# Optimization experiments

Hardware: AMD Instinct MI355X
Metric: run time of the kernel (lower is better)

The kernel has to match this reference:

```python
import jax, jax.numpy as jnp
import numpy as np

N, C, H, W = 64, 512, 32, 32
HID, NCLS = 240, 10


def setup_inputs() -> dict:
    key = jax.random.key(0)
    ks = jax.random.split(key, 6)
    d = {
        "x": jax.random.normal(ks[0], (N, C, H, W), jnp.float32),
        "bn1_g": jnp.ones((C,), jnp.float32),
        "bn1_b": jnp.zeros((C,), jnp.float32),
        "bn1_m": jnp.zeros((C,), jnp.float32),
        "bn1_v": jnp.ones((C,), jnp.float32),
        "conv1_w": jax.random.normal(ks[1], (C, C, 3, 3), jnp.float32) * 0.02,
        "bn2_g": jnp.ones((C,), jnp.float32),
        "bn2_b": jnp.zeros((C,), jnp.float32),
        "bn2_m": jnp.zeros((C,), jnp.float32),
        "bn2_v": jnp.ones((C,), jnp.float32),
        "conv2_w": jax.random.normal(ks[2], (C, C, 3, 3), jnp.float32) * 0.02,
        "fc1_w": jax.random.normal(ks[3], (HID, C), jnp.float32) * 0.05,
        "fc1_b": jnp.zeros((HID,), jnp.float32),
        "fc2_w": jax.random.normal(ks[4], (NCLS, HID), jnp.float32) * 0.05,
        "fc2_b": jnp.zeros((NCLS,), jnp.float32),
    }
    return d


def _bn(x, g, b, m, v, eps=1e-5):
    # eval-mode BatchNorm2d, NCHW
    inv = g / jnp.sqrt(v + eps)
    return x * inv[None, :, None, None] + (b - m * inv)[None, :, None, None]


def _conv3(x, w):
    return jax.lax.conv_general_dilated(
        x, w, window_strides=(1, 1), padding="SAME",
        dimension_numbers=("NCHW", "OIHW", "NCHW"))


def _probe(feat, fc1_w, fc1_b, fc2_w, fc2_b):
    # Global_Avg_Flatten -> Linear -> Softplus(beta=5) -> Linear
    g = feat.mean(axis=(2, 3))                       # (N, C)
    h = jax.nn.softplus(5.0 * (g @ fc1_w.T + fc1_b)) / 5.0  # (N, HID)
    return h @ fc2_w.T + fc2_b                       # (N, NCLS)


def _get_mask(feat, fc1_w, fc1_b, fc2_w, fc2_b):
    # eval branch: sum of top-1 + top-2 logits, grad wrt (detached) feat
    feat_sg = jax.lax.stop_gradient(feat)

    def logit_sum(f_):
        logits = _probe(f_, fc1_w, fc1_b, fc2_w, fc2_b)
        idx = jax.lax.top_k(logits, 2)[1]            # (N, 2) int indices
        return jnp.take_along_axis(logits, idx, axis=1).sum()

    g = jax.grad(logit_sum)(feat_sg)                 # (N, C, H, W)
    # adaptive_avg_pool2d(.,1)*H*W == spatial sum
    s = g.sum(axis=(2, 3))                           # (N, C)
    m = jax.nn.softmax(s, axis=1) * 2.0
    return m[:, :, None, None]


def reference(x, bn1_g, bn1_b, bn1_m, bn1_v, conv1_w,
              bn2_g, bn2_b, bn2_m, bn2_v, conv2_w,
              fc1_w, fc1_b, fc2_w, fc2_b):
    out1 = jax.nn.relu(_bn(x, bn1_g, bn1_b, bn1_m, bn1_v))  # equalInOut path
    mask = _get_mask(out1, fc1_w, fc1_b, fc2_w, fc2_b)
    pred_probe = _probe(out1, fc1_w, fc1_b, fc2_w, fc2_b)
    masked = out1 * mask
    h = jax.nn.relu(_bn(_conv3(masked, conv1_w), bn2_g, bn2_b, bn2_m, bn2_v))
    h = _conv3(h, conv2_w)
    out = x + h
    return (out, pred_probe)
```

## Files before the change

kernel.cpp:

```cpp
#include <hip/hip_runtime.h>
#include <stdint.h>

typedef __bf16 bf16x8 __attribute__((ext_vector_type(8)));
typedef float f32x4v __attribute__((ext_vector_type(4)));

typedef __attribute__((address_space(1))) const void gconst_t;
typedef __attribute__((address_space(3))) void lds_t;

#define GLL16(gp, sp) __builtin_amdgcn_global_load_lds((gconst_t*)(uintptr_t)(gp), (lds_t*)(uintptr_t)(sp), 16, 0, 0)

__device__ __forceinline__ unsigned short f2bf(float f) {
  unsigned int u = __float_as_uint(f);
  u = (u + 0x7FFFu + ((u >> 16) & 1u)) >> 16;
  return (unsigned short)u;
}
__device__ __forceinline__ float bf2f(unsigned int b) {
  return __uint_as_float(b << 16);
}

#define SPP 1156

__global__ __launch_bounds__(512) void bnprep(
    const float* __restrict__ g1, const float* __restrict__ b1,
    const float* __restrict__ m1, const float* __restrict__ v1,
    const float* __restrict__ g2, const float* __restrict__ b2,
    const float* __restrict__ m2, const float* __restrict__ v2,
    float* __restrict__ bnp) {
  int t = threadIdx.x;
  float i1 = g1[t] * rsqrtf(v1[t] + 1e-5f);
  bnp[t] = i1;
  bnp[512 + t] = b1[t] - m1[t] * i1;
  float i2 = g2[t] * rsqrtf(v2[t] + 1e-5f);
  bnp[1024 + t] = i2;
  bnp[1536 + t] = b2[t] - m2[t] * i2;
}

__global__ __launch_bounds__(256) void ring_zero(unsigned short* __restrict__ Ap,
                                                 unsigned short* __restrict__ Hp) {
  const int n = blockIdx.y;
  const int p = blockIdx.x * 4 + (threadIdx.x >> 6);
  const int lane = threadIdx.x & 63;
  int y, x;
  if (p < 34) { y = 0; x = p; }
  else if (p < 68) { y = 33; x = p - 34; }
  else if (p < 100) { y = p - 67; x = 0; }
  else { y = p - 99; x = 33; }
  const uint4 z = {0u, 0u, 0u, 0u};
  const size_t off = ((size_t)((n * 34 + y) * 34 + x)) * 512 + lane * 8;
  *(uint4*)(Ap + off) = z;
  *(uint4*)(Hp + off) = z;
}

__global__ __launch_bounds__(256) void wtrans(const float* __restrict__ w1, const float* __restrict__ w2,
                                              unsigned short* __restrict__ w1t, unsigned short* __restrict__ w2t) {
  unsigned e = blockIdx.x * 256u + threadIdx.x;
  if (e >= 4718592u) return;
  const float* w = (e < 2359296u) ? w1 : w2;
  unsigned short* o = (e < 2359296u) ? w1t : w2t;
  unsigned r = (e < 2359296u) ? e : (e - 2359296u);
  unsigned ci = r & 511u, co = (r >> 9) & 511u, tt = r >> 18;
  o[r] = f2bf(w[(co * 512u + ci) * 9u + tt]);
}

__global__ __launch_bounds__(256) void bn1_relu_stage(const float* __restrict__ x, const float* __restrict__ bnp,
                                                      unsigned short* __restrict__ Ap, float* __restrict__ partial) {
  int bid = blockIdx.x;
  int n = bid >> 6, ciblk = (bid >> 3) & 7, yblk = bid & 7;
  int ci0 = ciblk * 64, y0 = yblk * 4;
  int t = threadIdx.x;
  __shared__ __align__(16) float vals[64 * 128];
  __shared__ float ivs[64], bbs[64];
  if (t < 64) { ivs[t] = bnp[ci0 + t]; bbs[t] = bnp[512 + ci0 + t]; }
  __syncthreads();
#pragma unroll
  for (int i = 0; i < 8; ++i) {
    int f4 = i * 256 + t;
    int cil = f4 >> 5, xq = f4 & 31;
    const float* src = x + ((size_t)(n * 512 + ci0 + cil)) * 1024 + y0 * 32 + xq * 4;
    f32x4v v = *(const f32x4v*)src;
    float iv = ivs[cil], bb = bbs[cil];
    f32x4v r;
    r[0] = fmaxf(fmaf(v[0], iv, bb), 0.f);
    r[1] = fmaxf(fmaf(v[1], iv, bb), 0.f);
    r[2] = fmaxf(fmaf(v[2], iv, bb), 0.f);
    r[3] = fmaxf(fmaf(v[3], iv, bb), 0.f);
    *(f32x4v*)&vals[cil * 128 + xq * 4] = r;
  }
  __syncthreads();
  {
    int cil = t >> 2, q = t & 3;
    float s = 0.f;
#pragma unroll
    for (int j = 0; j < 32; ++j) s += vals[cil * 128 + q * 32 + j];
    s += __shfl_xor(s, 1);
    s += __shfl_xor(s, 2);
    if (q == 0) partial[((size_t)n * 512 + ci0 + cil) * 8 + yblk] = s;
  }
  {
    int yx = t >> 1, half = t & 1;
    int y = y0 + (yx >> 5), xx = yx & 31;
    unsigned short* dp = Ap + ((size_t)((n * 34 + y + 1) * 34 + (xx + 1))) * 512 + ci0 + half * 32;
    unsigned wrd[16];
#pragma unroll
    for (int j = 0; j < 16; ++j) {
      unsigned lo = f2bf(vals[(half * 32 + 2 * j) * 128 + yx]);
      unsigned hi = f2bf(vals[(half * 32 + 2 * j + 1) * 128 + yx]);
      wrd[j] = lo | (hi << 16);
    }
#pragma unroll
    for (int k = 0; k < 4; ++k) {
      uint4 u;
      u.x = wrd[k * 4]; u.y = wrd[k * 4 + 1]; u.z = wrd[k * 4 + 2]; u.w = wrd[k * 4 + 3];
      *(uint4*)(dp + k * 8) = u;
    }
  }
}

__global__ __launch_bounds__(256) void probe_mask(const float* __restrict__ partial,
                                                  const float* __restrict__ fc1w, const float* __restrict__ fc1b,
                                                  const float* __restrict__ fc2w, const float* __restrict__ fc2b,
                                                  float* __restrict__ maskp, float* __restrict__ probeout) {
  int n = blockIdx.x, t = threadIdx.x;
  int lane = t & 63, wv = t >> 6;
  __shared__ float gl[512], sl[512], zl[240], hl[240], dzl[240], logl[10], red[4];
  __shared__ int idx2[2];
  for (int c = t; c < 512; c += 256) {
    const float* pp = partial + ((size_t)n * 512 + c) * 8;
    float s = 0.f;
#pragma unroll
    for (int j = 0; j < 8; ++j) s += pp[j];
    gl[c] = s * (1.f / 1024.f);
  }
  __syncthreads();
  if (t < 240) {
    float z = fc1b[t];
    const float* wr = fc1w + t * 512;
    for (int c = 0; c < 512; ++c) z = fmaf(gl[c], wr[c], z);
    zl[t] = z;
    float u = 5.f * z;
    float sp = (u > 20.f) ? u : log1pf(expf(u));
    hl[t] = sp * 0.2f;
  }
  __syncthreads();
  if (t < 10) {
    float L = fc2b[t];
    const float* wr = fc2w + t * 240;
    for (int h = 0; h < 240; ++h) L = fmaf(hl[h], wr[h], L);
    logl[t] = L;
    probeout[n * 10 + t] = L;
  }
  __syncthreads();
  if (t == 0) {
    float b1v = -1e30f, b2v = -1e30f; int i1 = 0, i2 = 0;
    for (int j = 0; j < 10; ++j) {
      float v = logl[j];
      if (v > b1v) { b2v = b1v; i2 = i1; b1v = v; i1 = j; }
      else if (v > b2v) { b2v = v; i2 = j; }
    }
    idx2[0] = i1; idx2[1] = i2;
  }
  __syncthreads();
  if (t < 240) {
    float dh = fc2w[idx2[0] * 240 + t] + fc2w[idx2[1] * 240 + t];
    float u = 5.f * zl[t];
    float sg = 1.f / (1.f + expf(-u));
    dzl[t] = dh * sg;
  }
  __syncthreads();
  for (int c = t; c < 512; c += 256) {
    float s = 0.f;
    for (int h = 0; h < 240; ++h) s = fmaf(dzl[h], fc1w[h * 512 + c], s);
    sl[c] = s;
  }
  __syncthreads();
  float m = fmaxf(sl[t], sl[t + 256]);
#pragma unroll
  for (int o = 32; o > 0; o >>= 1) m = fmaxf(m, __shfl_xor(m, o));
  if (lane == 0) red[wv] = m;
  __syncthreads();
  float mx = fmaxf(fmaxf(red[0], red[1]), fmaxf(red[2], red[3]));
  float e0 = expf(sl[t] - mx), e1 = expf(sl[t + 256] - mx);
  float sum = e0 + e1;
#pragma unroll
  for (int o = 32; o > 0; o >>= 1) sum += __shfl_xor(sum, o);
  __syncthreads();
  if (lane == 0) red[wv] = sum;
  __syncthreads();
  float inv = 2.f / (red[0] + red[1] + red[2] + red[3]);
  maskp[(size_t)n * 512 + t] = e0 * inv;
  maskp[(size_t)n * 512 + t + 256] = e1 * inv;
}

__global__ __launch_bounds__(256) void apply_mask(unsigned short* __restrict__ Ap, const float* __restrict__ maskp) {
  int n = blockIdx.y;
  size_t off = (size_t)n * (SPP * 512) + (size_t)blockIdx.x * 2048 + threadIdx.x * 8;
  int ci0 = (int)(threadIdx.x * 8) & 511;
  uint4 v = *(uint4*)(Ap + off);
  const float* mp = maskp + n * 512 + ci0;
  unsigned r0, r1;
  r0 = f2bf(bf2f(v.x & 0xFFFFu) * mp[0]); r1 = f2bf(bf2f(v.x >> 16) * mp[1]); v.x = r0 | (r1 << 16);
  r0 = f2bf(bf2f(v.y & 0xFFFFu) * mp[2]); r1 = f2bf(bf2f(v.y >> 16) * mp[3]); v.y = r0 | (r1 << 16);
  r0 = f2bf(bf2f(v.z & 0xFFFFu) * mp[4]); r1 = f2bf(bf2f(v.z >> 16) * mp[5]); v.z = r0 | (r1 << 16);
  r0 = f2bf(bf2f(v.w & 0xFFFFu) * mp[6]); r1 = f2bf(bf2f(v.w >> 16) * mp[7]); v.w = r0 | (r1 << 16);
  *(uint4*)(Ap + off) = v;
}

#define LT(M) ((l4 ^ (((M) + l7) & 7)) << 4)

#define RD_A2(QM, H, TAP) do {                                                \
  const int _S0 = ((QM) * 2 + (H) + (TAP) / 3) * 34 + (TAP) % 3;              \
  const int _l = l15x128 + LT(_S0 & 7);                                       \
  const char* _p = ldsAW + _S0 * 128;                                         \
  a2[0][0] = *(const bf16x8*)(_p + _l);                                       \
  a2[0][1] = *(const bf16x8*)(_p + (_l ^ 64));                                \
  a2[1][0] = *(const bf16x8*)(_p + 2048 + _l);                                \
  a2[1][1] = *(const bf16x8*)(_p + 2048 + (_l ^ 64));                         \
} while (0)

#define RD_B(BUF) do {                                                        \
  const char* _pb = ldsb + 49152 + (BUF) * 16384;                             \
  b[0][0] = *(const bf16x8*)(_pb + bRdC);                                     \
  b[0][1] = *(const bf16x8*)(_pb + (bRdC ^ 64));                              \
  b[1][0] = *(const bf16x8*)(_pb + 2048 + bRdC);                              \
  b[1][1] = *(const bf16x8*)(_pb + 2048 + (bRdC ^ 64));                       \
} while (0)

#define ST_B(BUF, BP) do {                                                    \
  GLL16((BP) + bOff0,         ldsb + 49152 + (BUF) * 16384 + tb);             \
  GLL16((BP) + bOff0 + 32768, ldsb + 49152 + (BUF) * 16384 + 8192 + tb);      \
} while (0)

#define ST_A3(AP) do {                                                        \
  GLL16((AP) + aOff0,          ldsb + tb);                                    \
  GLL16((AP) + aOff0 + 32768,  ldsb + 8192 + tb);                             \
  GLL16((AP) + aOff0 + 65536,  ldsb + 16384 + tb);                            \
  GLL16((AP) + aOff0 + 98304,  ldsb + 24576 + tb);                            \
  GLL16((AP) + aOff0 + 131072, ldsb + 32768 + tb);                            \
  GLL16((AP) + aOff0 + 163840, ldsb + 40960 + tb);                            \
} while (0)

#define MFMA8(QM, H) do {                                                     \
  _Pragma("unroll") for (int m = 0; m < 2; ++m)                               \
  _Pragma("unroll") for (int n2 = 0; n2 < 2; ++n2) {                          \
    acc[QM][(H) * 2 + m][n2] = __builtin_amdgcn_mfma_f32_16x16x32_bf16(       \
        a2[m][0], b[n2][0], acc[QM][(H) * 2 + m][n2], 0, 0, 0);               \
    acc[QM][(H) * 2 + m][n2] = __builtin_amdgcn_mfma_f32_16x16x32_bf16(       \
        a2[m][1], b[n2][1], acc[QM][(H) * 2 + m][n2], 0, 0, 0); }             \
} while (0)

#define BARR __builtin_amdgcn_s_barrier()
#define LGKM0 do { asm volatile("s_waitcnt lgkmcnt(0)" ::: "memory");         \
                   __builtin_amdgcn_sched_barrier(0); } while (0)
#define VM0 asm volatile("s_waitcnt vmcnt(0)" ::: "memory")
#define PRIO1 __builtin_amdgcn_s_setprio(1)
#define PRIO0 __builtin_amdgcn_s_setprio(0)

#define TAPSTEP(TAP, PAR) do {                                                \
  const unsigned short* _bpn;                                                 \
  if ((TAP) < 8) _bpn = Wt + (size_t)((TAP) + 1) * 262144 + k8 * 64;          \
  else           _bpn = (k8 < 7) ? Wt + (size_t)(k8 + 1) * 64                 \
                                 : Wt + (size_t)8 * 262144 + 7 * 64;          \
  ST_B((((TAP) + (PAR)) & 1) ^ 1, _bpn);                                      \
  RD_B(((TAP) + (PAR)) & 1);                                                  \
  RD_A2(0, 0, TAP); PRIO1; MFMA8(0, 0); PRIO0;                                \
  RD_A2(0, 1, TAP); PRIO1; MFMA8(0, 1); PRIO0;                                \
  RD_A2(1, 0, TAP); PRIO1; MFMA8(1, 0); PRIO0;                                \
  if ((TAP) < 8) {                                                            \
    RD_A2(1, 1, TAP); PRIO1; MFMA8(1, 1); PRIO0;                              \
    VM0; LGKM0; BARR;                                                         \
  } else {                                                                    \
    RD_A2(1, 1, TAP);                                                         \
    LGKM0; BARR;                                                              \
    if (k8 < 7) { ST_A3(Ag + (size_t)(k8 + 1) * 64); }                        \
    PRIO1; MFMA8(1, 1); PRIO0;                                                \
    VM0; BARR;                                                                \
  }                                                                           \
} while (0)

#define TAP9(PAR)                                                             \
  TAPSTEP(0, PAR); TAPSTEP(1, PAR); TAPSTEP(2, PAR);                          \
  TAPSTEP(3, PAR); TAPSTEP(4, PAR); TAPSTEP(5, PAR);                          \
  TAPSTEP(6, PAR); TAPSTEP(7, PAR); TAPSTEP(8, PAR);

template <int MODE>
__global__ __attribute__((amdgpu_flat_work_group_size(512, 512), amdgpu_waves_per_eu(4, 4)))
void conv256(
    const unsigned short* __restrict__ Ain,
    const unsigned short* __restrict__ Wt,
    const float* __restrict__ bnp,
    unsigned short* __restrict__ Hout,
    const float* __restrict__ xres,
    float* __restrict__ outp) {
  __shared__ __align__(16) char ldsb[81920];

  const int t = threadIdx.x;
  const int lane = t & 63;
  const int wv = t >> 6;
  const int wm = wv >> 2;
  const int wn = wv & 3;

  const int bid = blockIdx.x;
  const int logical = (bid & 7) * 128 + (bid >> 3);
  const int nt = logical & 3, mt = logical >> 2;
  const int n = mt >> 2, yblk = mt & 3;
  const int co0 = nt * 128;

  const unsigned short* Ag = Ain + (size_t)n * (SPP * 512);

  const int kq8 = ((t & 7) ^ ((t >> 3) & 7)) * 8;
  const int aOff0 = (yblk * 272 + (t >> 3)) * 512 + kq8;
  const int bOff0 = (co0 + (t >> 3)) * 512 + kq8;
  const int tb = t * 16;
  const int l4 = lane >> 4, l7 = lane & 7;
  const int l15x128 = (lane & 15) * 128;
  const char* ldsAW = ldsb + wm * 17408;
  const int bRdC = (wn * 32 + (lane & 15)) * 128 + (((lane >> 4) ^ (lane & 7)) << 4);

  bf16x8 a2[2][2];
  bf16x8 b[2][2];
  f32x4v acc[2][4][2];
  const f32x4v zero = {0.f, 0.f, 0.f, 0.f};
#pragma unroll
  for (int qm = 0; qm < 2; ++qm)
#pragma unroll
    for (int mi = 0; mi < 4; ++mi)
#pragma unroll
      for (int ni = 0; ni < 2; ++ni) acc[qm][mi][ni] = zero;

  {
    ST_A3(Ag);
    ST_B(0, Wt);
    VM0; BARR;
  }

  for (int k2 = 0; k2 < 4; ++k2) {
    {
      const int k8 = 2 * k2;
      TAP9(0)
    }
    {
      const int k8 = 2 * k2 + 1;
      TAP9(1)
    }
  }
  VM0;
  __syncthreads();

  if constexpr (MODE == 1) {
#pragma unroll
    for (int ni = 0; ni < 2; ++ni) {
      const int cog = co0 + wn * 32 + ni * 16 + (lane & 15);
      const float iv = bnp[1024 + cog];
      const float bb = bnp[1536 + cog];
#pragma unroll
      for (int qm = 0; qm < 2; ++qm)
#pragma unroll
        for (int mi = 0; mi < 4; ++mi)
#pragma unroll
          for (int r = 0; r < 4; ++r) {
            const int row = wm * 128 + qm * 64 + mi * 16 + (lane >> 4) * 4 + r;
            const int y = yblk * 8 + (row >> 5), xx = row & 31;
            const float v = fmaxf(fmaf(acc[qm][mi][ni][r], iv, bb), 0.f);
            Hout[((size_t)((n * 34 + y + 1) * 34 + (xx + 1))) * 512 + cog] = f2bf(v);
          }
    }
  } else {
    float* sm = (float*)ldsb;
    const int spat0 = yblk * 256;
#pragma unroll 1
    for (int h = 0; h < 4; ++h) {
      if (wn == h) {
#pragma unroll
        for (int ni = 0; ni < 2; ++ni)
#pragma unroll
          for (int qm = 0; qm < 2; ++qm)
#pragma unroll
            for (int mi = 0; mi < 4; ++mi)
#pragma unroll
              for (int r = 0; r < 4; ++r)
                sm[(ni * 16 + (lane & 15)) * 264 +
                   wm * 128 + qm * 64 + mi * 16 + (lane >> 4) * 4 + r] = acc[qm][mi][ni][r];
      }
      __syncthreads();
#pragma unroll
      for (int j = 0; j < 4; ++j) {
        const int c = j * 512 + t;
        const int cc = c >> 6, px = (c & 63) * 4;
        f32x4v v = *(const f32x4v*)&sm[cc * 264 + px];
        const int cog = co0 + h * 32 + cc;
        const size_t o = ((size_t)(n * 512 + cog)) * 1024 + spat0 + px;
        const f32x4v xr = *(const f32x4v*)(xres + o);
        v = v + xr;
        *(f32x4v*)(outp + o) = v;
      }
      __syncthreads();
    }
  }
}

extern "C" void kernel_launch(void* const* d_in, const int* in_sizes, int n_in,
                              void* d_out, int out_size, void* d_ws, size_t ws_size,
                              hipStream_t stream) {
  (void)in_sizes; (void)n_in; (void)out_size; (void)ws_size;
  const float* x    = (const float*)d_in[0];
  const float* bn1g = (const float*)d_in[1];
  const float* bn1b = (const float*)d_in[2];
  const float* bn1m = (const float*)d_in[3];
  const float* bn1v = (const float*)d_in[4];
  const float* w1   = (const float*)d_in[5];
  const float* bn2g = (const float*)d_in[6];
  const float* bn2b = (const float*)d_in[7];
  const float* bn2m = (const float*)d_in[8];
  const float* bn2v = (const float*)d_in[9];
  const float* w2   = (const float*)d_in[10];
  const float* fc1w = (const float*)d_in[11];
  const float* fc1b = (const float*)d_in[12];
  const float* fc2w = (const float*)d_in[13];
  const float* fc2b = (const float*)d_in[14];

  float* out = (float*)d_out;
  float* probeo = out + (size_t)64 * 512 * 32 * 32;

  char* ws = (char*)d_ws;
  unsigned short* Ap  = (unsigned short*)(ws);
  unsigned short* Hp  = (unsigned short*)(ws + 75759616);
  unsigned short* W1t = (unsigned short*)(ws + 151519232);
  unsigned short* W2t = (unsigned short*)(ws + 156237824);
  float* partial      = (float*)(ws + 160956416);
  float* maskp        = (float*)(ws + 162004992);
  float* bnp          = (float*)(ws + 162136064);

  bnprep<<<1, 512, 0, stream>>>(bn1g, bn1b, bn1m, bn1v, bn2g, bn2b, bn2m, bn2v, bnp);
  ring_zero<<<dim3(33, 64), 256, 0, stream>>>(Ap, Hp);
  wtrans<<<18432, 256, 0, stream>>>(w1, w2, W1t, W2t);
  bn1_relu_stage<<<4096, 256, 0, stream>>>(x, bnp, Ap, partial);
  probe_mask<<<64, 256, 0, stream>>>(partial, fc1w, fc1b, fc2w, fc2b, maskp, probeo);
  apply_mask<<<dim3(289, 64), 256, 0, stream>>>(Ap, maskp);
  conv256<1><<<1024, 512, 0, stream>>>(Ap, W1t, bnp, Hp, nullptr, nullptr);
  conv256<2><<<1024, 512, 0, stream>>>(Hp, W2t, bnp, nullptr, x, out);
}
```

Baseline: 578.4 us.

## Switch conv MFMA tiling from 16x16x32 to 32x32x16 bf16 instructions

The implicit-GEMM conv kernel now uses 32x32x16 bf16 MFMAs with four 16-wide accumulators per wave instead of sixteen 16x16 tiles. Each wave covers four image rows of 32 pixels by 32 output channels, and one B fragment is reused across four A fragments per K step. The aim is fewer LDS reads per MFMA and fewer, larger matrix instructions. The LDS swizzle, accumulator layout and both epilogues are rewritten to match. The transpose scratch stride changes to 265 floats, which breaks 16-byte alignment of the vector reads in the residual epilogue.

```diff
diff --git a/kernel.cpp b/kernel.cpp
--- a/kernel.cpp
+++ b/kernel.cpp
@@ -3,6 +3,7 @@
 
 typedef __bf16 bf16x8 __attribute__((ext_vector_type(8)));
 typedef float f32x4v __attribute__((ext_vector_type(4)));
+typedef float f32x16 __attribute__((ext_vector_type(16)));
 
 typedef __attribute__((address_space(1))) const void gconst_t;
 typedef __attribute__((address_space(3))) void lds_t;
@@ -205,25 +206,12 @@
   *(uint4*)(Ap + off) = v;
 }
 
-#define LT(M) ((l4 ^ (((M) + l7) & 7)) << 4)
-
-#define RD_A2(QM, H, TAP) do {                                                \
-  const int _S0 = ((QM) * 2 + (H) + (TAP) / 3) * 34 + (TAP) % 3;              \
-  const int _l = l15x128 + LT(_S0 & 7);                                       \
-  const char* _p = ldsAW + _S0 * 128;                                         \
-  a2[0][0] = *(const bf16x8*)(_p + _l);                                       \
-  a2[0][1] = *(const bf16x8*)(_p + (_l ^ 64));                                \
-  a2[1][0] = *(const bf16x8*)(_p + 2048 + _l);                                \
-  a2[1][1] = *(const bf16x8*)(_p + 2048 + (_l ^ 64));                         \
-} while (0)
-
-#define RD_B(BUF) do {                                                        \
-  const char* _pb = ldsb + 49152 + (BUF) * 16384;                             \
-  b[0][0] = *(const bf16x8*)(_pb + bRdC);                                     \
-  b[0][1] = *(const bf16x8*)(_pb + (bRdC ^ 64));                              \
-  b[1][0] = *(const bf16x8*)(_pb + 2048 + bRdC);                              \
-  b[1][1] = *(const bf16x8*)(_pb + 2048 + (bRdC ^ 64));                       \
-} while (0)
+#define BARR __builtin_amdgcn_s_barrier()
+#define LGKM0 do { asm volatile("s_waitcnt lgkmcnt(0)" ::: "memory");         \
+                   __builtin_amdgcn_sched_barrier(0); } while (0)
+#define VM0 asm volatile("s_waitcnt vmcnt(0)" ::: "memory")
+#define PRIO1 __builtin_amdgcn_s_setprio(1)
+#define PRIO0 __builtin_amdgcn_s_setprio(0)
 
 #define ST_B(BUF, BP) do {                                                    \
   GLL16((BP) + bOff0,         ldsb + 49152 + (BUF) * 16384 + tb);             \
@@ -239,48 +227,69 @@
   GLL16((AP) + aOff0 + 163840, ldsb + 40960 + tb);                            \
 } while (0)
 
-#define MFMA8(QM, H) do {                                                     \
-  _Pragma("unroll") for (int m = 0; m < 2; ++m)                               \
-  _Pragma("unroll") for (int n2 = 0; n2 < 2; ++n2) {                          \
-    acc[QM][(H) * 2 + m][n2] = __builtin_amdgcn_mfma_f32_16x16x32_bf16(       \
-        a2[m][0], b[n2][0], acc[QM][(H) * 2 + m][n2], 0, 0, 0);               \
-    acc[QM][(H) * 2 + m][n2] = __builtin_amdgcn_mfma_f32_16x16x32_bf16(       \
-        a2[m][1], b[n2][1], acc[QM][(H) * 2 + m][n2], 0, 0, 0); }             \
-} while (0)
-
-#define BARR __builtin_amdgcn_s_barrier()
-#define LGKM0 do { asm volatile("s_waitcnt lgkmcnt(0)" ::: "memory");         \
-                   __builtin_amdgcn_sched_barrier(0); } while (0)
-#define VM0 asm volatile("s_waitcnt vmcnt(0)" ::: "memory")
-#define PRIO1 __builtin_amdgcn_s_setprio(1)
-#define PRIO0 __builtin_amdgcn_s_setprio(0)
-
-#define TAPSTEP(TAP, PAR) do {                                                \
-  const unsigned short* _bpn;                                                 \
-  if ((TAP) < 8) _bpn = Wt + (size_t)((TAP) + 1) * 262144 + k8 * 64;          \
-  else           _bpn = (k8 < 7) ? Wt + (size_t)(k8 + 1) * 64                 \
-                                 : Wt + (size_t)8 * 262144 + 7 * 64;          \
+#define MFMA_KK(TAP, BUF, K) do {                                             \
+  const bf16x8 _bf = *(const bf16x8*)(ldsB + (BUF) * 16384 + (bT ^ ((K) << 5))); \
+  const int _Sa = ((TAP) / 3) * 34 + (TAP) % 3;                               \
+  const bf16x8 _a0 = *(const bf16x8*)(ldsAW + (_Sa + 0) * 128 + (aT[(_Sa + 0) & 7] ^ ((K) << 5)));   \
+  const bf16x8 _a1 = *(const bf16x8*)(ldsAW + (_Sa + 34) * 128 + (aT[(_Sa + 34) & 7] ^ ((K) << 5))); \
+  const bf16x8 _a2 = *(const bf16x8*)(ldsAW + (_Sa + 68) * 128 + (aT[(_Sa + 68) & 7] ^ ((K) << 5))); \
+  const bf16x8 _a3 = *(const bf16x8*)(ldsAW + (_Sa + 102) * 128 + (aT[(_Sa + 102) & 7] ^ ((K) << 5))); \
+  acc0 = __builtin_amdgcn_mfma_f32_32x32x16_bf16(_a0, _bf, acc0, 0, 0, 0);    \
+  acc1 = __builtin_amdgcn_mfma_f32_32x32x16_bf16(_a1, _bf, acc1, 0, 0, 0);    \
+  acc2 = __builtin_amdgcn_mfma_f32_32x32x16_bf16(_a2, _bf, acc2, 0, 0, 0);    \
+  acc3 = __builtin_amdgcn_mfma_f32_32x32x16_bf16(_a3, _bf, acc3, 0, 0, 0);    \
+} while (0)
+
+#define TS(TAP, PAR) do {                                                     \
+  const unsigned short* _bpn = Wt + (size_t)((TAP) + 1) * 262144 + k8 * 64;   \
   ST_B((((TAP) + (PAR)) & 1) ^ 1, _bpn);                                      \
-  RD_B(((TAP) + (PAR)) & 1);                                                  \
-  RD_A2(0, 0, TAP); PRIO1; MFMA8(0, 0); PRIO0;                                \
-  RD_A2(0, 1, TAP); PRIO1; MFMA8(0, 1); PRIO0;                                \
-  RD_A2(1, 0, TAP); PRIO1; MFMA8(1, 0); PRIO0;                                \
-  if ((TAP) < 8) {                                                            \
-    RD_A2(1, 1, TAP); PRIO1; MFMA8(1, 1); PRIO0;                              \
-    VM0; LGKM0; BARR;                                                         \
-  } else {                                                                    \
-    RD_A2(1, 1, TAP);                                                         \
+  PRIO1;                                                                      \
+  MFMA_KK(TAP, ((TAP) + (PAR)) & 1, 0);                                       \
+  MFMA_KK(TAP, ((TAP) + (PAR)) & 1, 1);                                       \
+  MFMA_KK(TAP, ((TAP) + (PAR)) & 1, 2);                                       \
+  MFMA_KK(TAP, ((TAP) + (PAR)) & 1, 3);                                       \
+  PRIO0;                                                                      \
+  VM0; LGKM0; BARR;                                                           \
+} while (0)
+
+#define TS_LAST(PAR) do {                                                     \
+  const unsigned short* _bpn = (k8 < 7) ? Wt + (size_t)(k8 + 1) * 64          \
+                                        : Wt + (size_t)8 * 262144 + 7 * 64;   \
+  ST_B(((8 + (PAR)) & 1) ^ 1, _bpn);                                          \
+  PRIO1;                                                                      \
+  MFMA_KK(8, (8 + (PAR)) & 1, 0);                                             \
+  MFMA_KK(8, (8 + (PAR)) & 1, 1);                                             \
+  MFMA_KK(8, (8 + (PAR)) & 1, 2);                                             \
+  PRIO0;                                                                      \
+  {                                                                           \
+    const int _Sa = 2 * 34 + 2;                                               \
+    const bf16x8 _bf = *(const bf16x8*)(ldsB + ((8 + (PAR)) & 1) * 16384 + (bT ^ (3 << 5))); \
+    const bf16x8 _a0 = *(const bf16x8*)(ldsAW + (_Sa + 0) * 128 + (aT[(_Sa + 0) & 7] ^ (3 << 5)));   \
+    const bf16x8 _a1 = *(const bf16x8*)(ldsAW + (_Sa + 34) * 128 + (aT[(_Sa + 34) & 7] ^ (3 << 5))); \
+    const bf16x8 _a2 = *(const bf16x8*)(ldsAW + (_Sa + 68) * 128 + (aT[(_Sa + 68) & 7] ^ (3 << 5))); \
+    const bf16x8 _a3 = *(const bf16x8*)(ldsAW + (_Sa + 102) * 128 + (aT[(_Sa + 102) & 7] ^ (3 << 5))); \
     LGKM0; BARR;                                                              \
     if (k8 < 7) { ST_A3(Ag + (size_t)(k8 + 1) * 64); }                        \
-    PRIO1; MFMA8(1, 1); PRIO0;                                                \
+    PRIO1;                                                                    \
+    acc0 = __builtin_amdgcn_mfma_f32_32x32x16_bf16(_a0, _bf, acc0, 0, 0, 0);  \
+    acc1 = __builtin_amdgcn_mfma_f32_32x32x16_bf16(_a1, _bf, acc1, 0, 0, 0);  \
+    acc2 = __builtin_amdgcn_mfma_f32_32x32x16_bf16(_a2, _bf, acc2, 0, 0, 0);  \
+    acc3 = __builtin_amdgcn_mfma_f32_32x32x16_bf16(_a3, _bf, acc3, 0, 0, 0);  \
+    PRIO0;                                                                    \
     VM0; BARR;                                                                \
   }                                                                           \
 } while (0)
 
 #define TAP9(PAR)                                                             \
-  TAPSTEP(0, PAR); TAPSTEP(1, PAR); TAPSTEP(2, PAR);                          \
-  TAPSTEP(3, PAR); TAPSTEP(4, PAR); TAPSTEP(5, PAR);                          \
-  TAPSTEP(6, PAR); TAPSTEP(7, PAR); TAPSTEP(8, PAR);
+  TS(0, PAR); TS(1, PAR); TS(2, PAR); TS(3, PAR);                             \
+  TS(4, PAR); TS(5, PAR); TS(6, PAR); TS(7, PAR); TS_LAST(PAR);
+
+#define EPI_T(ACC, MF) do {                                                   \
+  _Pragma("unroll") for (int r = 0; r < 16; ++r) {                            \
+    const int xx = (r & 3) + 8 * (r >> 2) + 4 * hi;                           \
+    sm[lx * 265 + ((wm * 4 + (MF)) * 32 + xx)] = ACC[r];                      \
+  }                                                                           \
+} while (0)
 
 template <int MODE>
 __global__ __attribute__((amdgpu_flat_work_group_size(512, 512), amdgpu_waves_per_eu(4, 4)))
@@ -291,13 +300,15 @@
     unsigned short* __restrict__ Hout,
     const float* __restrict__ xres,
     float* __restrict__ outp) {
-  __shared__ __align__(16) char ldsb[81920];
+  __shared__ __align__(128) char ldsb[81920];
 
   const int t = threadIdx.x;
   const int lane = t & 63;
   const int wv = t >> 6;
   const int wm = wv >> 2;
   const int wn = wv & 3;
+  const int lx = lane & 31;
+  const int hi = lane >> 5;
 
   const int bid = blockIdx.x;
   const int logical = (bid & 7) * 128 + (bid >> 3);
@@ -311,21 +322,19 @@
   const int aOff0 = (yblk * 272 + (t >> 3)) * 512 + kq8;
   const int bOff0 = (co0 + (t >> 3)) * 512 + kq8;
   const int tb = t * 16;
-  const int l4 = lane >> 4, l7 = lane & 7;
-  const int l15x128 = (lane & 15) * 128;
+
+  int aT[8];
+#pragma unroll
+  for (int m = 0; m < 8; ++m)
+    aT[m] = lx * 128 + ((hi ^ ((m + lx) & 7)) << 4);
+  const int bT = (wn * 32 + lx) * 128 + ((hi ^ (lx & 7)) << 4);
   const char* ldsAW = ldsb + wm * 17408;
-  const int bRdC = (wn * 32 + (lane & 15)) * 128 + (((lane >> 4) ^ (lane & 7)) << 4);
-
-  bf16x8 a2[2][2];
-  bf16x8 b[2][2];
-  f32x4v acc[2][4][2];
-  const f32x4v zero = {0.f, 0.f, 0.f, 0.f};
-#pragma unroll
-  for (int qm = 0; qm < 2; ++qm)
-#pragma unroll
-    for (int mi = 0; mi < 4; ++mi)
-#pragma unroll
-      for (int ni = 0; ni < 2; ++ni) acc[qm][mi][ni] = zero;
+  const char* ldsB = ldsb + 49152;
+
+  f32x16 acc0 = {0.f};
+  f32x16 acc1 = {0.f};
+  f32x16 acc2 = {0.f};
+  f32x16 acc3 = {0.f};
 
   {
     ST_A3(Ag);
@@ -347,46 +356,33 @@
   __syncthreads();
 
   if constexpr (MODE == 1) {
-#pragma unroll
-    for (int ni = 0; ni < 2; ++ni) {
-      const int cog = co0 + wn * 32 + ni * 16 + (lane & 15);
-      const float iv = bnp[1024 + cog];
-      const float bb = bnp[1536 + cog];
-#pragma unroll
-      for (int qm = 0; qm < 2; ++qm)
-#pragma unroll
-        for (int mi = 0; mi < 4; ++mi)
-#pragma unroll
-          for (int r = 0; r < 4; ++r) {
-            const int row = wm * 128 + qm * 64 + mi * 16 + (lane >> 4) * 4 + r;
-            const int y = yblk * 8 + (row >> 5), xx = row & 31;
-            const float v = fmaxf(fmaf(acc[qm][mi][ni][r], iv, bb), 0.f);
-            Hout[((size_t)((n * 34 + y + 1) * 34 + (xx + 1))) * 512 + cog] = f2bf(v);
-          }
-    }
+    const int cog = co0 + wn * 32 + lx;
+    const float iv = bnp[1024 + cog];
+    const float bb2 = bnp[1536 + cog];
+#define EPI1(ACC, MF) do {                                                    \
+    const int y = yblk * 8 + wm * 4 + (MF);                                   \
+    unsigned short* hb = Hout + ((size_t)((n * 34 + y + 1) * 34 + 1)) * 512 + cog; \
+    _Pragma("unroll") for (int r = 0; r < 16; ++r) {                          \
+      const int xx = (r & 3) + 8 * (r >> 2) + 4 * hi;                         \
+      hb[(size_t)xx * 512] = f2bf(fmaxf(fmaf(ACC[r], iv, bb2), 0.f));         \
+    }                                                                         \
+  } while (0)
+    EPI1(acc0, 0); EPI1(acc1, 1); EPI1(acc2, 2); EPI1(acc3, 3);
+#undef EPI1
   } else {
     float* sm = (float*)ldsb;
     const int spat0 = yblk * 256;
 #pragma unroll 1
     for (int h = 0; h < 4; ++h) {
       if (wn == h) {
-#pragma unroll
-        for (int ni = 0; ni < 2; ++ni)
-#pragma unroll
-          for (int qm = 0; qm < 2; ++qm)
-#pragma unroll
-            for (int mi = 0; mi < 4; ++mi)
-#pragma unroll
-              for (int r = 0; r < 4; ++r)
-                sm[(ni * 16 + (lane & 15)) * 264 +
-                   wm * 128 + qm * 64 + mi * 16 + (lane >> 4) * 4 + r] = acc[qm][mi][ni][r];
+        EPI_T(acc0, 0); EPI_T(acc1, 1); EPI_T(acc2, 2); EPI_T(acc3, 3);
       }
       __syncthreads();
 #pragma unroll
       for (int j = 0; j < 4; ++j) {
         const int c = j * 512 + t;
         const int cc = c >> 6, px = (c & 63) * 4;
-        f32x4v v = *(const f32x4v*)&sm[cc * 264 + px];
+        f32x4v v = *(const f32x4v*)&sm[cc * 265 + px];
         const int cog = co0 + h * 32 + cc;
         const size_t o = ((size_t)(n * 512 + cog)) * 1024 + spat0 + px;
         const f32x4v xr = *(const f32x4v*)(xres + o);
```

Result: slower. 655.7 us (+13.4%).
